# Optimization experiments

Hardware: AMD Instinct MI355X
Metric: run time of the kernel (lower is better)

## Reference

```python
import jax, jax.numpy as jnp
import numpy as np

D_MODEL = 2048
N_HEADS = 16
HEAD_DIM = D_MODEL // N_HEADS  # 128
B, S = 4, 2048


def setup_inputs() -> dict:
    key = jax.random.key(0)
    ks = jax.random.split(key, 7)
    scale = 1.0 / np.sqrt(D_MODEL)
    return {
        "x": jax.random.normal(ks[0], (B, S, D_MODEL), dtype=jnp.float32),
        "cos": jax.random.uniform(ks[1], (S, HEAD_DIM // 2), dtype=jnp.float32),
        "sin": jax.random.uniform(ks[2], (S, HEAD_DIM // 2), dtype=jnp.float32),
        "Wq": jax.random.normal(ks[3], (D_MODEL, D_MODEL), dtype=jnp.float32) * scale,
        "Wk": jax.random.normal(ks[4], (D_MODEL, D_MODEL), dtype=jnp.float32) * scale,
        "Wv": jax.random.normal(ks[5], (D_MODEL, D_MODEL), dtype=jnp.float32) * scale,
        "Wo": jax.random.normal(ks[6], (D_MODEL, D_MODEL), dtype=jnp.float32) * scale,
    }


def apply_rope(x, cos, sin):
    # x: [B, H, S, head_dim]; cos/sin: [S, half] (split-in-half RoPE)
    half = x.shape[-1] // 2
    x1, x2 = x[..., :half], x[..., half:]
    cos = cos[None, None, :, :].astype(x.dtype)
    sin = sin[None, None, :, :].astype(x.dtype)
    return jnp.concatenate([x1 * cos - x2 * sin, x1 * sin + x2 * cos], axis=-1)


def reference(x, cos, sin, Wq, Wk, Wv, Wo):
    Bx, Sx, _ = x.shape
    # nn.Linear: y = x @ W.T
    def proj(W):
        y = jnp.einsum("bsd,ed->bse", x, W)
        return y.reshape(Bx, Sx, N_HEADS, HEAD_DIM).transpose(0, 2, 1, 3)  # [B,H,S,hd]
    q = apply_rope(proj(Wq), cos, sin)
    k = apply_rope(proj(Wk), cos, sin)
    v = proj(Wv)
    scale = 1.0 / np.sqrt(HEAD_DIM)
    scores = jnp.einsum("bhqd,bhkd->bhqk", q, k) * scale  # [B,H,S,S]
    attn = jax.nn.softmax(scores, axis=-1)
    out = jnp.einsum("bhqk,bhkd->bhqd", attn, v)
    out = out.transpose(0, 2, 1, 3).reshape(Bx, Sx, D_MODEL)
    return jnp.einsum("bsd,ed->bse", out, Wo)
```

## Files before the change

kernel.cpp:

```cpp
#include <hip/hip_runtime.h>

typedef _Float16 half_t;
typedef __attribute__((ext_vector_type(8))) _Float16 half8;
typedef __attribute__((ext_vector_type(4))) _Float16 half4v;
typedef __attribute__((ext_vector_type(4))) float f32x4;

#define MFMA16(a,b,c) __builtin_amdgcn_mfma_f32_16x16x32_f16((a),(b),(c),0,0,0)

__device__ __forceinline__ void gld_lds16(const half_t* g, half_t* l){
    __builtin_amdgcn_global_load_lds((__attribute__((address_space(1))) void*)(g),
                                     (__attribute__((address_space(3))) void*)(l), 16, 0, 0);
}

__global__ __launch_bounds__(256) void cvt_k(const float* __restrict__ s, half_t* __restrict__ d, int n4){
    int i = blockIdx.x * 256 + threadIdx.x;
    if (i < n4){
        float4 v = ((const float4*)s)[i];
        half4v h = { (half_t)v.x, (half_t)v.y, (half_t)v.z, (half_t)v.w };
        ((half4v*)d)[i] = h;
    }
}

__global__ __launch_bounds__(256) void cvtw_k(const float* __restrict__ w0, const float* __restrict__ w1,
                                              const float* __restrict__ w2, const float* __restrict__ w3,
                                              half_t* __restrict__ dst){
    const float* srcs[4] = {w0, w1, w2, w3};
    const float* s = srcs[blockIdx.y];
    int i = blockIdx.x * 256 + threadIdx.x;
    float4 v = ((const float4*)s)[i];
    half4v h = { (half_t)v.x, (half_t)v.y, (half_t)v.z, (half_t)v.w };
    ((half4v*)(dst))[(size_t)blockIdx.y * 1048576 + i] = h;
}

#define VMWAIT_(n) asm volatile("s_waitcnt vmcnt(" #n ")" ::: "memory")
#define VMWAIT(n)  VMWAIT_(n)

#define STAGE8(hh) { \
    const int Tt2 = (hh) >> 2, jj2 = (hh) & 3; \
    half_t* db = smem + ((jj2 & 1) << 15) + ((Tt2 & 1) << 14) + ((jj2 >> 1) << 13); \
    const half_t* Gs = ((jj2 & 1) ? Bg : Ag) + Tt2*64 + ((jj2 >> 1) << 5); \
    gld_lds16(Gs + off0, db + d0); \
    gld_lds16(Gs + off1, db + d1); \
}

#define PHASE8(Tt, jj, hh, VMN) { \
    half_t* Ah = smem + (((Tt) & 1) << 14) + (((jj) >> 1) << 13); \
    half_t* Bh = Ah + 32768; \
    half8 af[4], bf[4]; \
    _Pragma("unroll") for (int x = 0; x < 4; x++) af[x] = *(const half8*)(Ah + (((jj)&1)*4 + x)*1024 + cA); \
    _Pragma("unroll") for (int y = 0; y < 4; y++) bf[y] = *(const half8*)(Bh + y*1024 + cB); \
    if ((hh) < 128) STAGE8(hh); \
    if ((jj) & 1) VMWAIT(VMN); \
    asm volatile("s_barrier" ::: "memory"); \
    __builtin_amdgcn_s_setprio(1); \
    _Pragma("unroll") for (int x = 0; x < 4; x++) \
      _Pragma("unroll") for (int y = 0; y < 4; y++) \
        acc[((jj)&1)*4 + x][y] = MFMA16(af[x], bf[y], acc[((jj)&1)*4 + x][y]); \
    __builtin_amdgcn_s_setprio(0); \
    __builtin_amdgcn_sched_barrier(0); \
    asm volatile("s_barrier" ::: "memory"); \
}

__global__ __launch_bounds__(512) void gemm8(const half_t* __restrict__ A, const half_t* __restrict__ B,
                                             half_t* __restrict__ Qw, half_t* __restrict__ Kw,
                                             half_t* __restrict__ Vt, float* __restrict__ Co, int kind){
    const int tid  = threadIdx.x;
    const int lane = tid & 63;
    const int w4   = lane >> 4;
    const int l15  = lane & 15;
    const int l7   = lane & 7;
    const int wav  = tid >> 6;
    const int wavM = wav >> 2;
    const int wnq  = wav & 3;

    const int nwg = gridDim.x;
    const int wg  = blockIdx.x;
    const int swz = (wg & 7) * (nwg >> 3) + (wg >> 3);
    const int bm  = swz & 31;
    const int bn  = swz >> 5;

    __shared__ __align__(16) half_t smem[65536];

    const half_t* Ag = A + (size_t)bm * 256 * 2048;
    const half_t* Bg = B + (size_t)bn * 256 * 2048;

    const int p0  = tid >> 3, q0 = tid & 7, c0 = q0 ^ (p0 & 7);
    const int off0 = (p0 + ((c0 >> 2) << 7)) * 2048 + ((c0 & 3) << 3);
    const int off1 = off0 + 131072;
    const int d0  = tid * 8, d1 = d0 + 4096;

    const int cA = l15*64 + (((w4 | (wavM << 2)) ^ l7) << 3);
    const int cB = ((wnq & 1)*64 + l15)*64 + (((w4 | ((wnq >> 1) << 2)) ^ l7) << 3);

    f32x4 acc[8][4] = {};

#pragma unroll
    for (int h = 0; h < 6; h++) STAGE8(h);
    VMWAIT(4);
    asm volatile("s_barrier" ::: "memory");

    for (int it = 0; it < 15; it++){
        const int h0 = it*8 + 6;
        PHASE8(2*it,   0, h0,     6); PHASE8(2*it,   1, h0 + 1, 6);
        PHASE8(2*it,   2, h0 + 2, 6); PHASE8(2*it,   3, h0 + 3, 6);
        PHASE8(2*it+1, 0, h0 + 4, 6); PHASE8(2*it+1, 1, h0 + 5, 6);
        PHASE8(2*it+1, 2, h0 + 6, 6); PHASE8(2*it+1, 3, h0 + 7, 6);
    }
    PHASE8(30, 0, 126, 6); PHASE8(30, 1, 127, 6);
    PHASE8(30, 2, 128, 6); PHASE8(30, 3, 129, 2);
    PHASE8(31, 0, 130, 0); PHASE8(31, 1, 131, 0);
    PHASE8(31, 2, 132, 0); PHASE8(31, 3, 133, 0);

    const int mB = bm*256 + wavM*128 + w4*4;
    const int nB = bn*256 + wnq*64 + l15;

    if (kind == 0){
#pragma unroll
        for (int mi = 0; mi < 8; mi++)
#pragma unroll
            for (int ni = 0; ni < 4; ni++){
                int n  = nB + ni*16;
                int which = n >> 11;
                int nb = n & 2047;
                int m0 = mB + mi*16;
                if (which < 2){
                    half_t* dst = which ? Kw : Qw;
#pragma unroll
                    for (int r = 0; r < 4; r++){
                        int m = m0 + r;
                        dst[(((size_t)(m >> 11)*16 + (nb >> 7))*2048 + (m & 2047))*128 + (nb & 127)] = (half_t)acc[mi][ni][r];
                    }
                } else {
                    half4v hv = {(half_t)acc[mi][ni][0], (half_t)acc[mi][ni][1],
                                 (half_t)acc[mi][ni][2], (half_t)acc[mi][ni][3]};
                    *(half4v*)(Vt + (((size_t)(m0 >> 11)*16 + (nb >> 7))*128 + (nb & 127))*2048 + (m0 & 2047)) = hv;
                }
            }
    } else {
#pragma unroll
        for (int mi = 0; mi < 8; mi++)
#pragma unroll
            for (int ni = 0; ni < 4; ni++){
                int n  = nB + ni*16;
                int m0 = mB + mi*16;
#pragma unroll
                for (int r = 0; r < 4; r++)
                    Co[(size_t)(m0 + r)*2048 + n] = acc[mi][ni][r];
            }
    }
}

__global__ __launch_bounds__(256) void rope_k(half_t* __restrict__ Qw, half_t* __restrict__ Kw,
                                              const float* __restrict__ cs, const float* __restrict__ sn){
    int t  = blockIdx.x * 256 + threadIdx.x;
    int d  = t & 63;
    int s  = (t >> 6) & 2047;
    int bh = t >> 17;
    float c  = cs[s*64 + d];
    float si = sn[s*64 + d];
    size_t base = ((size_t)bh*2048 + s)*128 + d;
    float q1 = (float)Qw[base], q2 = (float)Qw[base+64];
    Qw[base]    = (half_t)(q1*c - q2*si);
    Qw[base+64] = (half_t)(q1*si + q2*c);
    float k1 = (float)Kw[base], k2 = (float)Kw[base+64];
    Kw[base]    = (half_t)(k1*c - k2*si);
    Kw[base+64] = (half_t)(k1*si + k2*c);
}

__global__ __launch_bounds__(256, 2) void attn_k(const half_t* __restrict__ Q, const half_t* __restrict__ K,
                                                 const half_t* __restrict__ Vt, half_t* __restrict__ AO){
    const int tid  = threadIdx.x;
    const int lane = tid & 63;
    const int w    = lane >> 4;
    const int l15  = lane & 15;
    const int l7   = lane & 7;
    const int wav  = tid >> 6;
    const int bid  = blockIdx.x;
    const int qt   = (bid >> 3) & 15;
    const int bh   = (bid & 7) * 8 + (bid >> 7);

    __shared__ __align__(16) half_t smem[40960];
    half_t* Ps = smem + 32768 + wav*2048;
    half_t* Ob = smem + wav*4096;

    const float SSC = 0.08838834764831845f * 1.4426950408889634f;

    const half_t* Qb = Q + ((size_t)bh*2048 + qt*128 + wav*32)*128;
    half8 aq[2][4];
#pragma unroll
    for (int qi = 0; qi < 2; qi++)
#pragma unroll
        for (int ks = 0; ks < 4; ks++){
            half8 t = *(const half8*)(Qb + (qi*16 + l15)*128 + ks*32 + w*8);
            aq[qi][ks] = t * (half_t)SSC;
        }

    const half_t* Kbase = K  + (size_t)bh*2048*128;
    const half_t* Vbase = Vt + (size_t)bh*128*2048;

#pragma unroll
    for (int i = 0; i < 4; i++){
        int c = tid + i*256;
        int key = c >> 4, pc = c & 15;
        gld_lds16(Kbase + key*128 + ((pc ^ (key & 7)) << 3), smem + c*8);
    }
#pragma unroll
    for (int i = 0; i < 4; i++){
        int c = tid + i*256;
        int d = c >> 3, pc = c & 7;
        gld_lds16(Vbase + (size_t)d*2048 + ((pc ^ (d & 7)) << 3), smem + 16384 + c*8);
    }

    f32x4 oacc[8][2] = {};
    float m_[2] = {-1e30f, -1e30f};
    float l_[2] = {0.0f, 0.0f};

    for (int kt = 0; kt < 32; kt++){
        half_t* kb = smem + ((kt & 1) << 13);
        half_t* vb = smem + 16384 + ((kt & 1) << 13);

        if (kt < 31){
            const half_t* Kb = Kbase + (size_t)(kt + 1)*8192;
            const half_t* Vb = Vbase + (kt + 1)*64;
            half_t* kn = smem + (((kt + 1) & 1) << 13);
            half_t* vn = smem + 16384 + (((kt + 1) & 1) << 13);
#pragma unroll
            for (int i = 0; i < 4; i++){
                int c = tid + i*256;
                int key = c >> 4, pc = c & 15;
                gld_lds16(Kb + key*128 + ((pc ^ (key & 7)) << 3), kn + c*8);
            }
#pragma unroll
            for (int i = 0; i < 4; i++){
                int c = tid + i*256;
                int d = c >> 3, pc = c & 7;
                gld_lds16(Vb + (size_t)d*2048 + ((pc ^ (d & 7)) << 3), vn + c*8);
            }
            VMWAIT(8);
        } else {
            VMWAIT(0);
        }
        asm volatile("s_barrier" ::: "memory");

        f32x4 sacc[4][2] = {};
#pragma unroll
        for (int ks = 0; ks < 4; ks++){
#pragma unroll
            for (int t = 0; t < 4; t++){
                half8 kf = *(const half8*)(kb + (t*16 + l15)*128 + (((ks*4 + w) ^ l7) << 3));
                sacc[t][0] = MFMA16(kf, aq[0][ks], sacc[t][0]);
                sacc[t][1] = MFMA16(kf, aq[1][ks], sacc[t][1]);
            }
        }

#pragma unroll
        for (int qi = 0; qi < 2; qi++){
            float mx = sacc[0][qi][0];
#pragma unroll
            for (int t = 0; t < 4; t++)
#pragma unroll
                for (int r = 0; r < 4; r++) mx = fmaxf(mx, sacc[t][qi][r]);
            mx = fmaxf(mx, __shfl_xor(mx, 16));
            mx = fmaxf(mx, __shfl_xor(mx, 32));
            unsigned long long upd = __ballot(mx > m_[qi]);
            if (upd){
                float mn    = fmaxf(m_[qi], mx);
                float alpha = exp2f(m_[qi] - mn);
                m_[qi] = mn;
                l_[qi] *= alpha;
#pragma unroll
                for (int t = 0; t < 8; t++)
#pragma unroll
                    for (int r = 0; r < 4; r++) oacc[t][qi][r] *= alpha;
            }
            float mq = m_[qi];
            float sum = 0.0f;
#pragma unroll
            for (int t = 0; t < 4; t++){
                float p0 = exp2f(sacc[t][qi][0] - mq);
                float p1 = exp2f(sacc[t][qi][1] - mq);
                float p2 = exp2f(sacc[t][qi][2] - mq);
                float p3 = exp2f(sacc[t][qi][3] - mq);
                sum += (p0 + p1) + (p2 + p3);
                half4v hv = {(half_t)p0, (half_t)p1, (half_t)p2, (half_t)p3};
                *(half4v*)(Ps + (qi*16 + l15)*64 + (((t*2 + (w >> 1)) ^ l7) << 3) + (w & 1)*4) = hv;
            }
            sum += __shfl_xor(sum, 16);
            sum += __shfl_xor(sum, 32);
            l_[qi] += sum;
        }

#pragma unroll
        for (int c2 = 0; c2 < 2; c2++){
            half8 pf0 = *(const half8*)(Ps + l15*64        + (((c2*4 + w) ^ l7) << 3));
            half8 pf1 = *(const half8*)(Ps + (16 + l15)*64 + (((c2*4 + w) ^ l7) << 3));
#pragma unroll
            for (int t = 0; t < 8; t++){
                half8 vf = *(const half8*)(vb + (t*16 + l15)*64 + (((c2*4 + w) ^ l7) << 3));
                oacc[t][0] = MFMA16(vf, pf0, oacc[t][0]);
                oacc[t][1] = MFMA16(vf, pf1, oacc[t][1]);
            }
        }

        asm volatile("s_barrier" ::: "memory");
    }

    float inv[2] = {1.0f / l_[0], 1.0f / l_[1]};
#pragma unroll
    for (int t = 0; t < 8; t++)
#pragma unroll
        for (int qi = 0; qi < 2; qi++){
            int q  = qi*16 + l15;
            int c8 = t*2 + (w>>1);
            int pc = c8 ^ l7;
            half4v hv = {(half_t)(oacc[t][qi][0]*inv[qi]), (half_t)(oacc[t][qi][1]*inv[qi]),
                         (half_t)(oacc[t][qi][2]*inv[qi]), (half_t)(oacc[t][qi][3]*inv[qi])};
            *(half4v*)(Ob + q*128 + pc*8 + (w&1)*4) = hv;
        }
    const int b = bh >> 4, h = bh & 15;
#pragma unroll
    for (int it = 0; it < 8; it++){
        int q  = it*4 + w;
        half8 rd = *(const half8*)(Ob + q*128 + ((l15 ^ (q&7)) << 3));
        int s = qt*128 + wav*32 + q;
        *(half8*)(AO + ((size_t)(b*2048 + s))*2048 + h*128 + l15*8) = rd;
    }
}

extern "C" void kernel_launch(void* const* d_in, const int* in_sizes, int n_in,
                              void* d_out, int out_size, void* d_ws, size_t ws_size,
                              hipStream_t stream){
    const float* x  = (const float*)d_in[0];
    const float* cs = (const float*)d_in[1];
    const float* sn = (const float*)d_in[2];
    const float* Wq = (const float*)d_in[3];
    const float* Wk = (const float*)d_in[4];
    const float* Wv = (const float*)d_in[5];
    const float* Wo = (const float*)d_in[6];

    half_t* ws = (half_t*)d_ws;
    half_t* xh = ws;
    half_t* w4 = ws + (size_t)16777216;
    half_t* qw = ws + (size_t)33554432;
    half_t* kw = ws + (size_t)50331648;
    half_t* vt = ws + (size_t)67108864;
    half_t* ao = ws + (size_t)83886080;

    cvt_k<<<16384, 256, 0, stream>>>(x, xh, 4194304);
    cvtw_k<<<dim3(4096, 4), 256, 0, stream>>>(Wq, Wk, Wv, Wo, w4);

    gemm8<<<768, 512, 0, stream>>>(xh, w4, qw, kw, vt, nullptr, 0);
    rope_k<<<32768, 256, 0, stream>>>(qw, kw, cs, sn);
    attn_k<<<1024, 256, 0, stream>>>(qw, kw, vt, ao);
    gemm8<<<256, 512, 0, stream>>>(ao, w4 + 12582912, nullptr, nullptr, nullptr,
                                   (float*)d_out, 1);
}
```

Before: 685.8 us.

## Halve attention key tile for higher occupancy, vectorize RoPE, merge convert kernels

The attention kernel now processes 32-key tiles instead of 64, halving LDS use and raising the launch bound to 4 blocks per CU for more occupancy, with K/V/P swizzles adjusted to the narrower tiles. RoPE is vectorized so each thread handles 8 elements with 16-byte loads and stores, and it launches far fewer blocks. The two fp32-to-fp16 conversion kernels are merged into one launch. Smaller tiles double the loop iterations and barriers, and the tighter register budget could cause spills.

After: 762.0 us. 1.11x slower.

```diff
diff --git a/kernel.cpp b/kernel.cpp
--- a/kernel.cpp
+++ b/kernel.cpp
@@ -12,24 +12,25 @@
                                      (__attribute__((address_space(3))) void*)(l), 16, 0, 0);
 }
 
-__global__ __launch_bounds__(256) void cvt_k(const float* __restrict__ s, half_t* __restrict__ d, int n4){
-    int i = blockIdx.x * 256 + threadIdx.x;
-    if (i < n4){
-        float4 v = ((const float4*)s)[i];
+__global__ __launch_bounds__(256) void cvt_all(const float* __restrict__ x,
+                                               const float* __restrict__ w0, const float* __restrict__ w1,
+                                               const float* __restrict__ w2, const float* __restrict__ w3,
+                                               half_t* __restrict__ xh, half_t* __restrict__ w4){
+    int b = blockIdx.x;
+    if (b < 16384){
+        int i = b * 256 + threadIdx.x;
+        float4 v = ((const float4*)x)[i];
         half4v h = { (half_t)v.x, (half_t)v.y, (half_t)v.z, (half_t)v.w };
-        ((half4v*)d)[i] = h;
-    }
-}
-
-__global__ __launch_bounds__(256) void cvtw_k(const float* __restrict__ w0, const float* __restrict__ w1,
-                                              const float* __restrict__ w2, const float* __restrict__ w3,
-                                              half_t* __restrict__ dst){
-    const float* srcs[4] = {w0, w1, w2, w3};
-    const float* s = srcs[blockIdx.y];
-    int i = blockIdx.x * 256 + threadIdx.x;
-    float4 v = ((const float4*)s)[i];
-    half4v h = { (half_t)v.x, (half_t)v.y, (half_t)v.z, (half_t)v.w };
-    ((half4v*)(dst))[(size_t)blockIdx.y * 1048576 + i] = h;
+        ((half4v*)xh)[i] = h;
+    } else {
+        int wi   = b - 16384;
+        int widx = wi >> 12;
+        int i    = (wi & 4095) * 256 + threadIdx.x;
+        const float* srcs[4] = {w0, w1, w2, w3};
+        float4 v = ((const float4*)srcs[widx])[i];
+        half4v h = { (half_t)v.x, (half_t)v.y, (half_t)v.z, (half_t)v.w };
+        ((half4v*)w4)[(size_t)widx * 1048576 + i] = h;
+    }
 }
 
 #define VMWAIT_(n) asm volatile("s_waitcnt vmcnt(" #n ")" ::: "memory")
@@ -153,34 +154,50 @@
 __global__ __launch_bounds__(256) void rope_k(half_t* __restrict__ Qw, half_t* __restrict__ Kw,
                                               const float* __restrict__ cs, const float* __restrict__ sn){
     int t  = blockIdx.x * 256 + threadIdx.x;
-    int d  = t & 63;
-    int s  = (t >> 6) & 2047;
-    int bh = t >> 17;
-    float c  = cs[s*64 + d];
-    float si = sn[s*64 + d];
-    size_t base = ((size_t)bh*2048 + s)*128 + d;
-    float q1 = (float)Qw[base], q2 = (float)Qw[base+64];
-    Qw[base]    = (half_t)(q1*c - q2*si);
-    Qw[base+64] = (half_t)(q1*si + q2*c);
-    float k1 = (float)Kw[base], k2 = (float)Kw[base+64];
-    Kw[base]    = (half_t)(k1*c - k2*si);
-    Kw[base+64] = (half_t)(k1*si + k2*c);
-}
-
-__global__ __launch_bounds__(256, 2) void attn_k(const half_t* __restrict__ Q, const half_t* __restrict__ K,
+    int c8 = t & 7;
+    int s  = (t >> 3) & 2047;
+    int bh = t >> 14;
+    size_t base = ((size_t)bh*2048 + s)*128 + c8*8;
+    const float4* cp = (const float4*)(cs + s*64 + c8*8);
+    const float4* sp = (const float4*)(sn + s*64 + c8*8);
+    float4 c0 = cp[0], c1 = cp[1];
+    float4 s0 = sp[0], s1 = sp[1];
+    float c[8]  = {c0.x,c0.y,c0.z,c0.w,c1.x,c1.y,c1.z,c1.w};
+    float si[8] = {s0.x,s0.y,s0.z,s0.w,s1.x,s1.y,s1.z,s1.w};
+
+    half8 qlo = *(const half8*)(Qw + base), qhi = *(const half8*)(Qw + base + 64);
+    half8 klo = *(const half8*)(Kw + base), khi = *(const half8*)(Kw + base + 64);
+    half8 qlo_o, qhi_o, klo_o, khi_o;
+#pragma unroll
+    for (int j = 0; j < 8; j++){
+        float q1 = (float)qlo[j], q2 = (float)qhi[j];
+        qlo_o[j] = (half_t)(q1*c[j] - q2*si[j]);
+        qhi_o[j] = (half_t)(q1*si[j] + q2*c[j]);
+        float k1 = (float)klo[j], k2 = (float)khi[j];
+        klo_o[j] = (half_t)(k1*c[j] - k2*si[j]);
+        khi_o[j] = (half_t)(k1*si[j] + k2*c[j]);
+    }
+    *(half8*)(Qw + base)      = qlo_o;
+    *(half8*)(Qw + base + 64) = qhi_o;
+    *(half8*)(Kw + base)      = klo_o;
+    *(half8*)(Kw + base + 64) = khi_o;
+}
+
+__global__ __launch_bounds__(256, 4) void attn_k(const half_t* __restrict__ Q, const half_t* __restrict__ K,
                                                  const half_t* __restrict__ Vt, half_t* __restrict__ AO){
     const int tid  = threadIdx.x;
     const int lane = tid & 63;
     const int w    = lane >> 4;
     const int l15  = lane & 15;
     const int l7   = lane & 7;
+    const int l3   = lane & 3;
     const int wav  = tid >> 6;
     const int bid  = blockIdx.x;
     const int qt   = (bid >> 3) & 15;
     const int bh   = (bid & 7) * 8 + (bid >> 7);
 
-    __shared__ __align__(16) half_t smem[40960];
-    half_t* Ps = smem + 32768 + wav*2048;
+    __shared__ __align__(16) half_t smem[20480];
+    half_t* Ps = smem + 16384 + wav*1024;
     half_t* Ob = smem + wav*4096;
 
     const float SSC = 0.08838834764831845f * 1.4426950408889634f;
@@ -199,54 +216,54 @@
     const half_t* Vbase = Vt + (size_t)bh*128*2048;
 
 #pragma unroll
-    for (int i = 0; i < 4; i++){
+    for (int i = 0; i < 2; i++){
         int c = tid + i*256;
         int key = c >> 4, pc = c & 15;
         gld_lds16(Kbase + key*128 + ((pc ^ (key & 7)) << 3), smem + c*8);
     }
 #pragma unroll
-    for (int i = 0; i < 4; i++){
+    for (int i = 0; i < 2; i++){
         int c = tid + i*256;
-        int d = c >> 3, pc = c & 7;
-        gld_lds16(Vbase + (size_t)d*2048 + ((pc ^ (d & 7)) << 3), smem + 16384 + c*8);
+        int d = c >> 2, pv = c & 3;
+        gld_lds16(Vbase + (size_t)d*2048 + ((pv ^ (d & 3)) << 3), smem + 8192 + c*8);
     }
 
     f32x4 oacc[8][2] = {};
     float m_[2] = {-1e30f, -1e30f};
     float l_[2] = {0.0f, 0.0f};
 
-    for (int kt = 0; kt < 32; kt++){
-        half_t* kb = smem + ((kt & 1) << 13);
-        half_t* vb = smem + 16384 + ((kt & 1) << 13);
-
-        if (kt < 31){
-            const half_t* Kb = Kbase + (size_t)(kt + 1)*8192;
-            const half_t* Vb = Vbase + (kt + 1)*64;
-            half_t* kn = smem + (((kt + 1) & 1) << 13);
-            half_t* vn = smem + 16384 + (((kt + 1) & 1) << 13);
-#pragma unroll
-            for (int i = 0; i < 4; i++){
+    for (int kt = 0; kt < 64; kt++){
+        half_t* kb = smem + ((kt & 1) << 12);
+        half_t* vb = smem + 8192 + ((kt & 1) << 12);
+
+        if (kt < 63){
+            const half_t* Kb = Kbase + (size_t)(kt + 1)*4096;
+            const half_t* Vb = Vbase + (kt + 1)*32;
+            half_t* kn = smem + (((kt + 1) & 1) << 12);
+            half_t* vn = smem + 8192 + (((kt + 1) & 1) << 12);
+#pragma unroll
+            for (int i = 0; i < 2; i++){
                 int c = tid + i*256;
                 int key = c >> 4, pc = c & 15;
                 gld_lds16(Kb + key*128 + ((pc ^ (key & 7)) << 3), kn + c*8);
             }
 #pragma unroll
-            for (int i = 0; i < 4; i++){
+            for (int i = 0; i < 2; i++){
                 int c = tid + i*256;
-                int d = c >> 3, pc = c & 7;
-                gld_lds16(Vb + (size_t)d*2048 + ((pc ^ (d & 7)) << 3), vn + c*8);
-            }
-            VMWAIT(8);
+                int d = c >> 2, pv = c & 3;
+                gld_lds16(Vb + (size_t)d*2048 + ((pv ^ (d & 3)) << 3), vn + c*8);
+            }
+            VMWAIT(4);
         } else {
             VMWAIT(0);
         }
         asm volatile("s_barrier" ::: "memory");
 
-        f32x4 sacc[4][2] = {};
+        f32x4 sacc[2][2] = {};
 #pragma unroll
         for (int ks = 0; ks < 4; ks++){
 #pragma unroll
-            for (int t = 0; t < 4; t++){
+            for (int t = 0; t < 2; t++){
                 half8 kf = *(const half8*)(kb + (t*16 + l15)*128 + (((ks*4 + w) ^ l7) << 3));
                 sacc[t][0] = MFMA16(kf, aq[0][ks], sacc[t][0]);
                 sacc[t][1] = MFMA16(kf, aq[1][ks], sacc[t][1]);
@@ -257,7 +274,7 @@
         for (int qi = 0; qi < 2; qi++){
             float mx = sacc[0][qi][0];
 #pragma unroll
-            for (int t = 0; t < 4; t++)
+            for (int t = 0; t < 2; t++)
 #pragma unroll
                 for (int r = 0; r < 4; r++) mx = fmaxf(mx, sacc[t][qi][r]);
             mx = fmaxf(mx, __shfl_xor(mx, 16));
@@ -276,27 +293,26 @@
             float mq = m_[qi];
             float sum = 0.0f;
 #pragma unroll
-            for (int t = 0; t < 4; t++){
+            for (int t = 0; t < 2; t++){
                 float p0 = exp2f(sacc[t][qi][0] - mq);
                 float p1 = exp2f(sacc[t][qi][1] - mq);
                 float p2 = exp2f(sacc[t][qi][2] - mq);
                 float p3 = exp2f(sacc[t][qi][3] - mq);
                 sum += (p0 + p1) + (p2 + p3);
                 half4v hv = {(half_t)p0, (half_t)p1, (half_t)p2, (half_t)p3};
-                *(half4v*)(Ps + (qi*16 + l15)*64 + (((t*2 + (w >> 1)) ^ l7) << 3) + (w & 1)*4) = hv;
+                *(half4v*)(Ps + (qi*16 + l15)*32 + (((t*2 + (w >> 1)) ^ l3) << 3) + (w & 1)*4) = hv;
             }
             sum += __shfl_xor(sum, 16);
             sum += __shfl_xor(sum, 32);
             l_[qi] += sum;
         }
 
-#pragma unroll
-        for (int c2 = 0; c2 < 2; c2++){
-            half8 pf0 = *(const half8*)(Ps + l15*64        + (((c2*4 + w) ^ l7) << 3));
-            half8 pf1 = *(const half8*)(Ps + (16 + l15)*64 + (((c2*4 + w) ^ l7) << 3));
+        {
+            half8 pf0 = *(const half8*)(Ps + l15*32        + ((w ^ l3) << 3));
+            half8 pf1 = *(const half8*)(Ps + (16 + l15)*32 + ((w ^ l3) << 3));
 #pragma unroll
             for (int t = 0; t < 8; t++){
-                half8 vf = *(const half8*)(vb + (t*16 + l15)*64 + (((c2*4 + w) ^ l7) << 3));
+                half8 vf = *(const half8*)(vb + (t*16 + l15)*32 + ((w ^ l3) << 3));
                 oacc[t][0] = MFMA16(vf, pf0, oacc[t][0]);
                 oacc[t][1] = MFMA16(vf, pf1, oacc[t][1]);
             }
@@ -346,11 +362,10 @@
     half_t* vt = ws + (size_t)67108864;
     half_t* ao = ws + (size_t)83886080;
 
-    cvt_k<<<16384, 256, 0, stream>>>(x, xh, 4194304);
-    cvtw_k<<<dim3(4096, 4), 256, 0, stream>>>(Wq, Wk, Wv, Wo, w4);
+    cvt_all<<<32768, 256, 0, stream>>>(x, Wq, Wk, Wv, Wo, xh, w4);
 
     gemm8<<<768, 512, 0, stream>>>(xh, w4, qw, kw, vt, nullptr, 0);
-    rope_k<<<32768, 256, 0, stream>>>(qw, kw, cs, sn);
+    rope_k<<<4096, 256, 0, stream>>>(qw, kw, cs, sn);
     attn_k<<<1024, 256, 0, stream>>>(qw, kw, vt, ao);
     gemm8<<<256, 512, 0, stream>>>(ao, w4 + 12582912, nullptr, nullptr, nullptr,
                                    (float*)d_out, 1);
```
